# Performance work log

Hardware: AMD Instinct MI355X
Metric: run time of the kernel (lower is better)

Reference implementation:

```python
import jax, jax.numpy as jnp
import numpy as np


def setup_inputs() -> dict:
    key = jax.random.key(0)
    ks = jax.random.split(key, 10)
    B, C, H = 128, 768, 12
    d = C // H
    t_h = t_w = 8
    s_h = s_w = 16
    Nt = t_h * t_w * 2          # 128 template tokens
    Ns = s_h * s_w + 4          # 260 search tokens
    N = Nt + Ns                 # 388
    s = 0.02
    return {
        "x": jax.random.normal(ks[0], (B, N, C), jnp.float32),
        "mem": jax.random.normal(ks[1], (B, H, d, d), jnp.float32),
        "z": jnp.ones((B, H, d, 1), jnp.float32),
        "qkv_w": jax.random.normal(ks[2], (3 * C, C), jnp.float32) * s,
        "qkv_b": jnp.zeros((3 * C,), jnp.float32),
        "proj_w": jax.random.normal(ks[3], (C, C), jnp.float32) * s,
        "proj_b": jnp.zeros((C,), jnp.float32),
        "memk_w": jax.random.normal(ks[4], (C, C), jnp.float32) * s,
        "memk_b": jnp.zeros((C,), jnp.float32),
        "memv_w": jax.random.normal(ks[5], (C, C), jnp.float32) * s,
        "memv_b": jnp.zeros((C,), jnp.float32),
        "betas": jax.random.normal(ks[6], (1, H, 1, d), jnp.float32),
        "t_h": t_h, "t_w": t_w, "s_h": s_h, "s_w": s_w,
    }


def reference(x, mem, z, qkv_w, qkv_b, proj_w, proj_b,
              memk_w, memk_b, memv_w, memv_b, betas,
              t_h, t_w, s_h, s_w):
    B, N, C = x.shape
    H = betas.shape[1]
    d = C // H
    Nt = t_h * t_w * 2
    Ns = s_h * s_w + 4
    scale = 1.0 / jnp.sqrt(jnp.float32(d))

    qkv = x @ qkv_w.T + qkv_b                       # [B,N,3C]
    qkv = qkv.reshape(B, N, 3, C)
    q_f, k_f, v_f = qkv[:, :, 0], qkv[:, :, 1], qkv[:, :, 2]  # [B,N,C]

    def heads(t):  # [B,N,C] -> [B,H,N,d]
        return t.reshape(B, -1, H, d).transpose(0, 2, 1, 3)

    q, k, v = heads(q_f), heads(k_f), heads(v_f)

    # memory k/v projections act on the raw (C-dim) search split of k,v
    k_s_mem = heads(k_f[:, Nt:, :] @ memk_w.T + memk_b)  # [B,H,Ns,d]
    v_s_mem = heads(v_f[:, Nt:, :] @ memv_w.T + memv_b)  # [B,H,Ns,d]

    q_mt, q_s = q[:, :, :Nt], q[:, :, Nt:]
    k_mt = k[:, :, :Nt]
    v_mt = v[:, :, :Nt]

    # template self-attention (q_mt only attends to k_mt)
    attn_mt = jax.nn.softmax(jnp.einsum('bhqd,bhkd->bhqk', q_mt, k_mt) * scale, axis=-1)
    x_mt = jnp.einsum('bhqk,bhkd->bhqd', attn_mt, v_mt)          # [B,H,Nt,d]
    x_mt = x_mt.transpose(0, 2, 1, 3).reshape(B, Nt, C)

    # search attends to full sequence
    attn_s = jax.nn.softmax(jnp.einsum('bhqd,bhkd->bhqk', q_s, k) * scale, axis=-1)
    x_s = jnp.einsum('bhqk,bhkd->bhqd', attn_s, v)               # [B,H,Ns,d]

    # linear-attention memory read (ELU feature map)
    sigma_q = jax.nn.elu(q_s) + 1.0                              # [B,H,Ns,d]
    att_mem = (sigma_q @ mem) / (sigma_q @ z)                    # [B,H,Ns,d]

    # delta-rule memory update
    sigma_k = jax.nn.elu(k_s_mem) + 1.0                          # [B,H,Ns,d]
    zz = jnp.sum(sigma_k, axis=-2, keepdims=True).swapaxes(-2, -1)  # [B,H,d,1]
    pred = (sigma_k @ mem) / (sigma_k @ z)                       # [B,H,Ns,d]
    mem_new = mem + jnp.einsum('bhnd,bhne->bhde', sigma_k, v_s_mem - pred)
    z_new = z + zz

    beta = jax.nn.sigmoid(betas)                                 # [1,H,1,d]
    x_s = beta * att_mem + (1.0 - beta) * x_s
    x_s = x_s.transpose(0, 2, 1, 3).reshape(B, Ns, C)

    out = jnp.concatenate([x_mt, x_s], axis=1) @ proj_w.T + proj_b
    return out, mem_new, z_new
```

## Files before the change

### kernel.cpp

```cpp
#include <hip/hip_runtime.h>

typedef unsigned short u16;
typedef __attribute__((ext_vector_type(8))) short  vbf8;
typedef __attribute__((ext_vector_type(4))) float  vf4;

#define B_   128
#define N_   388
#define NT   128
#define NS   260
#define C_   768
#define H_   12
#define D_   64
#define K3   2304

#define QKV_LEN  114425856ll
#define KSM_LEN  25559040ll
#define CAT_LEN  38141952ll
#define MEM_LEN  6291456ll

#define SPS  288
#define SWT_LEN 28311552ll

#define WOFF_QKV  0ll
#define WOFF_MEMK 1769472ll
#define WOFF_MEMV 2359296ll
#define WOFF_PROJ 2949120ll
#define WTOT     3538944ll
__device__ __align__(16) u16 g_wbf[3538944];

__device__ __forceinline__ float bf2f(u16 u) {
    union { unsigned int i; float f; } v; v.i = ((unsigned int)u) << 16; return v.f;
}
__device__ __forceinline__ u16 f2bf(float f) {
    union { float f; unsigned int i; } v; v.f = f;
    unsigned int r = v.i + 0x7fffu + ((v.i >> 16) & 1u);
    return (u16)(r >> 16);
}
__device__ __forceinline__ float elu1(float x) { return x > 0.f ? x + 1.f : __expf(x); }

__device__ __forceinline__ void gload_lds16(const u16* g, u16* l) {
    __builtin_amdgcn_global_load_lds(
        (const __attribute__((address_space(1))) unsigned int*)g,
        (__attribute__((address_space(3))) unsigned int*)l, 16, 0, 0);
}

__global__ __launch_bounds__(256) void convert_bf16(
    const float* __restrict__ src, u16* __restrict__ dst, long long n)
{
    long long i0 = ((long long)blockIdx.x * 256 + threadIdx.x) * 8;
    long long stride = (long long)gridDim.x * 256 * 8;
    for (long long i = i0; i < n; i += stride) {
        float4 a = *(const float4*)(src + i);
        float4 b = *(const float4*)(src + i + 4);
        ushort4 u1; u1.x = f2bf(a.x); u1.y = f2bf(a.y); u1.z = f2bf(a.z); u1.w = f2bf(a.w);
        ushort4 u2; u2.x = f2bf(b.x); u2.y = f2bf(b.y); u2.z = f2bf(b.z); u2.w = f2bf(b.w);
        *(ushort4*)(dst + i)     = u1;
        *(ushort4*)(dst + i + 4) = u2;
    }
}

__global__ __launch_bounds__(256) void convert_wbf_all(
    const float* __restrict__ s0, const float* __restrict__ s1,
    const float* __restrict__ s2, const float* __restrict__ s3)
{
    long long i = ((long long)blockIdx.x * 256 + threadIdx.x) * 8;
    if (i >= WTOT) return;
    const float* src; long long off;
    if (i < WOFF_MEMK)      { src = s0; off = i; }
    else if (i < WOFF_MEMV) { src = s1; off = i - WOFF_MEMK; }
    else if (i < WOFF_PROJ) { src = s2; off = i - WOFF_MEMV; }
    else                    { src = s3; off = i - WOFF_PROJ; }
    float4 a = *(const float4*)(src + off);
    float4 b = *(const float4*)(src + off + 4);
    ushort4 u1; u1.x = f2bf(a.x); u1.y = f2bf(a.y); u1.z = f2bf(a.z); u1.w = f2bf(a.w);
    ushort4 u2; u2.x = f2bf(b.x); u2.y = f2bf(b.y); u2.z = f2bf(b.z); u2.w = f2bf(b.w);
    *(ushort4*)(g_wbf + i)     = u1;
    *(ushort4*)(g_wbf + i + 4) = u2;
}

__global__ __launch_bounds__(256) void memT_kernel(
    const float* __restrict__ memin, u16* __restrict__ memT)
{
    __shared__ float ml[64 * 65];
    int bh = blockIdx.x, t = threadIdx.x;
    const float* src = memin + (long long)bh * 4096;
#pragma unroll
    for (int i = 0; i < 16; i++) {
        int idx = i * 256 + t;
        ml[(idx >> 6) * 65 + (idx & 63)] = src[idx];
    }
    __syncthreads();
    u16* dst = memT + (long long)bh * 4096;
#pragma unroll
    for (int i = 0; i < 16; i++) {
        int o = i * 256 + t;
        int dout = o >> 6, din = o & 63;
        dst[o] = f2bf(ml[din * 65 + dout]);
    }
}

template<int CF32>
__global__ __launch_bounds__(256) void gemm_mfma(
    const u16* __restrict__ A, long long off0, int rows_per_b,
    long long stride_b, long long stride_r,
    long long w_off, const float* __restrict__ bias,
    void* __restrict__ Cv, int Nout, int nbx)
{
    __shared__ __align__(16) u16 lds[2][2][4096];

    const u16* W = g_wbf + w_off;
    int t = threadIdx.x;

    int wg = blockIdx.x;
    wg = (wg & 7) * ((int)gridDim.x >> 3) + (wg >> 3);
    int m0 = (wg / nbx) * 128;
    int n0 = (wg % nbx) * 128;

    int lane = t & 63, w = t >> 6;
    int w512 = w * 512;

    int srow  = t >> 2;
    int scol  = (((t & 3) ^ ((t >> 3) & 3))) * 8;
    long long aoff0, aoff1;
    {
        int g1 = m0 + srow, g2 = g1 + 64;
        int b1 = g1 / rows_per_b, j1 = g1 - b1 * rows_per_b;
        int b2 = g2 / rows_per_b, j2 = g2 - b2 * rows_per_b;
        aoff0 = off0 + (long long)b1 * stride_b + (long long)j1 * stride_r + scol;
        aoff1 = off0 + (long long)b2 * stride_b + (long long)j2 * stride_r + scol;
    }
    const u16* wp0 = W + (long long)(n0 + srow) * 768 + scol;
    const u16* wp1 = W + (long long)(n0 + srow + 64) * 768 + scol;

    int lr = lane & 15, kg = lane >> 4;
    int wm = w >> 1, wn = w & 1;
    int aslot = (kg ^ ((lr >> 1) & 3)) * 8;
    int abase = (wm * 64 + lr) * 32 + aslot;
    int bbase = (wn * 64 + lr) * 32 + aslot;

    vf4 acc[4][4];
#pragma unroll
    for (int i = 0; i < 4; i++)
#pragma unroll
        for (int j = 0; j < 4; j++) acc[i][j] = vf4{0.f, 0.f, 0.f, 0.f};

    auto stage = [&](int buf, int kt) {
        gload_lds16(A + aoff0 + kt, &lds[buf][0][w512]);
        gload_lds16(A + aoff1 + kt, &lds[buf][0][2048 + w512]);
        gload_lds16(wp0 + kt,       &lds[buf][1][w512]);
        gload_lds16(wp1 + kt,       &lds[buf][1][2048 + w512]);
    };

    stage(0, 0);
    __syncthreads();

    int cur = 0;
    for (int kt = 0; kt < 768; kt += 32) {
        if (kt != 736) stage(cur ^ 1, kt + 32);

        vbf8 af[4], bf[4];
#pragma unroll
        for (int f = 0; f < 4; f++) {
            af[f] = *(const vbf8*)&lds[cur][0][abase + f * 512];
            bf[f] = *(const vbf8*)&lds[cur][1][bbase + f * 512];
        }
#pragma unroll
        for (int i = 0; i < 4; i++)
#pragma unroll
            for (int j = 0; j < 4; j++)
                acc[i][j] = __builtin_amdgcn_mfma_f32_16x16x32_bf16(
                    af[i], bf[j], acc[i][j], 0, 0, 0);

        __syncthreads();
        cur ^= 1;
    }

    if (!CF32) {
        u16* ct = &lds[0][0][0];
#pragma unroll
        for (int i = 0; i < 4; i++)
#pragma unroll
            for (int j = 0; j < 4; j++) {
                int col = wn * 64 + j * 16 + lr;
                float bb = bias[n0 + col];
#pragma unroll
                for (int r = 0; r < 4; r++)
                    ct[(wm * 64 + i * 16 + kg * 4 + r) * 128 + col] =
                        f2bf(acc[i][j][r] + bb);
            }
        __syncthreads();
        int col0 = (t & 15) * 8;
#pragma unroll
        for (int rr = 0; rr < 8; rr++) {
            int row_l = rr * 16 + (t >> 4);
            vbf8 v = *(const vbf8*)&ct[row_l * 128 + col0];
            *(vbf8*)((u16*)Cv + (long long)(m0 + row_l) * Nout + n0 + col0) = v;
        }
    } else {
        float* cf = (float*)&lds[0][0][0];
#pragma unroll
        for (int p = 0; p < 2; p++) {
            if (wm == p) {
#pragma unroll
                for (int i = 0; i < 4; i++)
#pragma unroll
                    for (int j = 0; j < 4; j++) {
                        int col = wn * 64 + j * 16 + lr;
                        float bb = bias[n0 + col];
#pragma unroll
                        for (int r = 0; r < 4; r++)
                            cf[(i * 16 + kg * 4 + r) * 128 + col] =
                                acc[i][j][r] + bb;
                    }
            }
            __syncthreads();
            int col0 = (t & 15) * 8;
#pragma unroll
            for (int rr = 0; rr < 4; rr++) {
                int row_l = rr * 16 + (t >> 4);
                float4 v0 = *(const float4*)&cf[row_l * 128 + col0];
                float4 v1 = *(const float4*)&cf[row_l * 128 + col0 + 4];
                float* dst = (float*)Cv + (long long)(m0 + p * 64 + row_l) * Nout + n0 + col0;
                *(float4*)dst = v0;
                *(float4*)(dst + 4) = v1;
            }
            __syncthreads();
        }
    }
}

#define SKP 416
#define VTS 424
__global__ __launch_bounds__(512) void attn_s_mfma(
    const u16* __restrict__ qkv, const u16* __restrict__ memT,
    const float* __restrict__ zin, const float* __restrict__ betas,
    u16* __restrict__ concat)
{
    __shared__ __align__(16) u16 Kl[SKP * 64];
    __shared__ __align__(16) u16 Vt[64 * VTS];
    __shared__ __align__(16) u16 Pl[8][16 * 40];
    __shared__ float red[8][16];

    int bh = blockIdx.x;
    int b = bh / H_, h = bh % H_;
    int t = threadIdx.x, lane = t & 63, w = t >> 6;
    int lr = lane & 15, q4 = lane >> 4;

    {
        int key0 = t >> 3;
        int d0 = (t & 7) * 8;
        for (int kp = 0; kp < SKP; kp += 64) {
            int key = kp + key0;
            if (key < SKP) {
                vbf8 kv, vv;
#pragma unroll
                for (int u = 0; u < 8; u++) { ((short*)&kv)[u] = 0; ((short*)&vv)[u] = 0; }
                if (key < N_) {
                    const u16* base = qkv + ((long long)(b * N_ + key)) * K3 + h * D_;
                    kv = *(const vbf8*)(base + C_ + d0);
                    vv = *(const vbf8*)(base + 2 * C_ + d0);
                }
                *(vbf8*)((char*)Kl + ((key * 128 + d0 * 2) ^ ((key & 7) << 4))) = kv;
#pragma unroll
                for (int u = 0; u < 8; u++) Vt[(d0 + u) * VTS + key] = ((u16*)&vv)[u];
            }
        }
    }
    __syncthreads();

    const float* zp = zin + bh * 64;
    const u16* mtb = memT + (long long)bh * 4096;

    for (int s = w; s < 17; s += 8) {
        int qtok = NT + s * 16 + lr;
        if (qtok > N_ - 1) qtok = N_ - 1;
        const u16* qbase = qkv + ((long long)(b * N_ + qtok)) * K3 + h * D_;
        vbf8 qf0 = *(const vbf8*)(qbase + q4 * 8);
        vbf8 qf1 = *(const vbf8*)(qbase + 32 + q4 * 8);

        vbf8 qs0, qs1;
#pragma unroll
        for (int j = 0; j < 8; j++) {
            ((u16*)&qs0)[j] = f2bf(bf2f(((u16*)&qf0)[j]) * 0.125f);
            ((u16*)&qs1)[j] = f2bf(bf2f(((u16*)&qf1)[j]) * 0.125f);
        }

        vf4 S[13][2];
#pragma unroll
        for (int kt = 0; kt < 13; kt++) {
#pragma unroll
            for (int ks = 0; ks < 2; ks++) {
                int krow = kt * 32 + ks * 16 + lr;
                int swz = (krow & 7) << 4;
                vbf8 b0 = *(const vbf8*)((char*)Kl + ((krow * 128 + q4 * 16) ^ swz));
                vbf8 b1 = *(const vbf8*)((char*)Kl + ((krow * 128 + 64 + q4 * 16) ^ swz));
                vf4 z4 = vf4{0.f, 0.f, 0.f, 0.f};
                vf4 sv = __builtin_amdgcn_mfma_f32_16x16x32_bf16(qs0, b0, z4, 0, 0, 0);
                S[kt][ks] = __builtin_amdgcn_mfma_f32_16x16x32_bf16(qs1, b1, sv, 0, 0, 0);
            }
        }
#pragma unroll
        for (int ks = 0; ks < 2; ks++)
#pragma unroll
            for (int r = 0; r < 4; r++)
                if (ks * 16 + lr >= 4) S[12][ks][r] = -1e30f;

        float mx[4];
#pragma unroll
        for (int r = 0; r < 4; r++) mx[r] = S[0][0][r];
#pragma unroll
        for (int kt = 0; kt < 13; kt++)
#pragma unroll
            for (int ks = 0; ks < 2; ks++)
#pragma unroll
                for (int r = 0; r < 4; r++) mx[r] = fmaxf(mx[r], S[kt][ks][r]);
#pragma unroll
        for (int off = 1; off <= 8; off <<= 1)
#pragma unroll
            for (int r = 0; r < 4; r++) mx[r] = fmaxf(mx[r], __shfl_xor(mx[r], off));

        float l[4] = {0.f, 0.f, 0.f, 0.f};
#pragma unroll
        for (int kt = 0; kt < 13; kt++)
#pragma unroll
            for (int ks = 0; ks < 2; ks++)
#pragma unroll
                for (int r = 0; r < 4; r++) {
                    float p = __expf(S[kt][ks][r] - mx[r]);
                    S[kt][ks][r] = p;
                    l[r] += p;
                }
#pragma unroll
        for (int off = 1; off <= 8; off <<= 1)
#pragma unroll
            for (int r = 0; r < 4; r++) l[r] += __shfl_xor(l[r], off);

        vf4 accO[4];
#pragma unroll
        for (int dc = 0; dc < 4; dc++) accO[dc] = vf4{0.f, 0.f, 0.f, 0.f};
#pragma unroll
        for (int kt = 0; kt < 13; kt++) {
            u16* pw = Pl[w];
#pragma unroll
            for (int ks = 0; ks < 2; ks++)
#pragma unroll
                for (int r = 0; r < 4; r++)
                    pw[(q4 * 4 + r) * 40 + ks * 16 + lr] = f2bf(S[kt][ks][r]);
            vbf8 pf = *(const vbf8*)&Pl[w][lr * 40 + q4 * 8];
#pragma unroll
            for (int dc = 0; dc < 4; dc++) {
                vbf8 vf_ = *(const vbf8*)&Vt[(dc * 16 + lr) * VTS + kt * 32 + q4 * 8];
                accO[dc] = __builtin_amdgcn_mfma_f32_16x16x32_bf16(pf, vf_, accO[dc], 0, 0, 0);
            }
        }

        float invl[4];
#pragma unroll
        for (int r = 0; r < 4; r++) invl[r] = 1.f / l[r];

        vbf8 sq0, sq1;
        float dpart = 0.f;
#pragma unroll
        for (int j = 0; j < 8; j++) {
            float s0 = elu1(bf2f(((u16*)&qf0)[j]));
            float s1 = elu1(bf2f(((u16*)&qf1)[j]));
            ((u16*)&sq0)[j] = f2bf(s0);
            ((u16*)&sq1)[j] = f2bf(s1);
            dpart += s0 * zp[q4 * 8 + j] + s1 * zp[32 + q4 * 8 + j];
        }
        dpart += __shfl_xor(dpart, 16);
        dpart += __shfl_xor(dpart, 32);
        if (q4 == 0) red[w][lr] = dpart;

        vf4 am[4];
#pragma unroll
        for (int dc = 0; dc < 4; dc++) {
            vbf8 b0 = *(const vbf8*)(mtb + (dc * 16 + lr) * 64 + q4 * 8);
            vbf8 b1 = *(const vbf8*)(mtb + (dc * 16 + lr) * 64 + 32 + q4 * 8);
            vf4 z4 = vf4{0.f, 0.f, 0.f, 0.f};
            vf4 a = __builtin_amdgcn_mfma_f32_16x16x32_bf16(sq0, b0, z4, 0, 0, 0);
            am[dc] = __builtin_amdgcn_mfma_f32_16x16x32_bf16(sq1, b1, a, 0, 0, 0);
        }
        float den[4];
#pragma unroll
        for (int r = 0; r < 4; r++) den[r] = 1.f / red[w][q4 * 4 + r];

#pragma unroll
        for (int dc = 0; dc < 4; dc++) {
            float bb = betas[h * D_ + dc * 16 + lr];
            float beta = 1.f / (1.f + __expf(-bb));
#pragma unroll
            for (int r = 0; r < 4; r++) {
                int qs = s * 16 + q4 * 4 + r;
                if (qs < NS) {
                    float o = beta * (am[dc][r] * den[r]) +
                              (1.f - beta) * (accO[dc][r] * invl[r]);
                    concat[((long long)(b * N_ + NT + qs)) * C_ + h * D_ + dc * 16 + lr] = f2bf(o);
                }
            }
        }
    }
}

#define MTS 136
__global__ __launch_bounds__(512) void attn_mt_mfma(
    const u16* __restrict__ qkv, u16* __restrict__ concat)
{
    __shared__ __align__(16) u16 Kl[NT * 64];
    __shared__ __align__(16) u16 Vt[64 * MTS];
    __shared__ __align__(16) u16 Pl[8][16 * 40];

    int bh = blockIdx.x;
    int b = bh / H_, h = bh % H_;
    int t = threadIdx.x, lane = t & 63, w = t >> 6;
    int lr = lane & 15, q4 = lane >> 4;

    {
        int key0 = t >> 3;
        int d0 = (t & 7) * 8;
#pragma unroll
        for (int kp = 0; kp < NT; kp += 64) {
            int key = kp + key0;
            const u16* base = qkv + ((long long)(b * N_ + key)) * K3 + h * D_;
            vbf8 kv = *(const vbf8*)(base + C_ + d0);
            vbf8 vv = *(const vbf8*)(base + 2 * C_ + d0);
            *(vbf8*)((char*)Kl + ((key * 128 + d0 * 2) ^ ((key & 7) << 4))) = kv;
#pragma unroll
            for (int u = 0; u < 8; u++) Vt[(d0 + u) * MTS + key] = ((u16*)&vv)[u];
        }
    }
    __syncthreads();

    int qtok = w * 16 + lr;
    const u16* qbase = qkv + ((long long)(b * N_ + qtok)) * K3 + h * D_;
    vbf8 qf0 = *(const vbf8*)(qbase + q4 * 8);
    vbf8 qf1 = *(const vbf8*)(qbase + 32 + q4 * 8);
    vbf8 qs0, qs1;
#pragma unroll
    for (int j = 0; j < 8; j++) {
        ((u16*)&qs0)[j] = f2bf(bf2f(((u16*)&qf0)[j]) * 0.125f);
        ((u16*)&qs1)[j] = f2bf(bf2f(((u16*)&qf1)[j]) * 0.125f);
    }

    vf4 S[4][2];
#pragma unroll
    for (int kt = 0; kt < 4; kt++) {
#pragma unroll
        for (int ks = 0; ks < 2; ks++) {
            int krow = kt * 32 + ks * 16 + lr;
            int swz = (krow & 7) << 4;
            vbf8 b0 = *(const vbf8*)((char*)Kl + ((krow * 128 + q4 * 16) ^ swz));
            vbf8 b1 = *(const vbf8*)((char*)Kl + ((krow * 128 + 64 + q4 * 16) ^ swz));
            vf4 z4 = vf4{0.f, 0.f, 0.f, 0.f};
            vf4 sv = __builtin_amdgcn_mfma_f32_16x16x32_bf16(qs0, b0, z4, 0, 0, 0);
            S[kt][ks] = __builtin_amdgcn_mfma_f32_16x16x32_bf16(qs1, b1, sv, 0, 0, 0);
        }
    }

    float mx[4];
#pragma unroll
    for (int r = 0; r < 4; r++) mx[r] = S[0][0][r];
#pragma unroll
    for (int kt = 0; kt < 4; kt++)
#pragma unroll
        for (int ks = 0; ks < 2; ks++)
#pragma unroll
            for (int r = 0; r < 4; r++) mx[r] = fmaxf(mx[r], S[kt][ks][r]);
#pragma unroll
    for (int off = 1; off <= 8; off <<= 1)
#pragma unroll
        for (int r = 0; r < 4; r++) mx[r] = fmaxf(mx[r], __shfl_xor(mx[r], off));

    float l[4] = {0.f, 0.f, 0.f, 0.f};
#pragma unroll
    for (int kt = 0; kt < 4; kt++)
#pragma unroll
        for (int ks = 0; ks < 2; ks++)
#pragma unroll
            for (int r = 0; r < 4; r++) {
                float p = __expf(S[kt][ks][r] - mx[r]);
                S[kt][ks][r] = p;
                l[r] += p;
            }
#pragma unroll
    for (int off = 1; off <= 8; off <<= 1)
#pragma unroll
        for (int r = 0; r < 4; r++) l[r] += __shfl_xor(l[r], off);

    vf4 accO[4];
#pragma unroll
    for (int dc = 0; dc < 4; dc++) accO[dc] = vf4{0.f, 0.f, 0.f, 0.f};
#pragma unroll
    for (int kt = 0; kt < 4; kt++) {
        u16* pw = Pl[w];
#pragma unroll
        for (int ks = 0; ks < 2; ks++)
#pragma unroll
            for (int r = 0; r < 4; r++)
                pw[(q4 * 4 + r) * 40 + ks * 16 + lr] = f2bf(S[kt][ks][r]);
        vbf8 pf = *(const vbf8*)&Pl[w][lr * 40 + q4 * 8];
#pragma unroll
        for (int dc = 0; dc < 4; dc++) {
            vbf8 vf_ = *(const vbf8*)&Vt[(dc * 16 + lr) * MTS + kt * 32 + q4 * 8];
            accO[dc] = __builtin_amdgcn_mfma_f32_16x16x32_bf16(pf, vf_, accO[dc], 0, 0, 0);
        }
    }

    float invl[4];
#pragma unroll
    for (int r = 0; r < 4; r++) invl[r] = 1.f / l[r];

    int qt0 = w * 16;
#pragma unroll
    for (int dc = 0; dc < 4; dc++)
#pragma unroll
        for (int r = 0; r < 4; r++) {
            int row = qt0 + q4 * 4 + r;
            concat[((long long)(b * N_ + row)) * C_ + h * D_ + dc * 16 + lr] =
                f2bf(accO[dc][r] * invl[r]);
        }
}

__global__ __launch_bounds__(512) void sigma_pred_mfma(
    const u16* __restrict__ ksm, const u16* __restrict__ vsm,
    const u16* __restrict__ memT, const float* __restrict__ zin,
    u16* __restrict__ sigT, u16* __restrict__ wT,
    float* __restrict__ z_out)
{
    __shared__ u16 sigLDS[8][64][18];
    __shared__ u16 wLDS[8][64][18];
    __shared__ float red[8][16];
    __shared__ float zpart[8][64];
    __shared__ float zlds[64];

    int bh = blockIdx.x;
    int b = bh / H_, h = bh % H_;
    int t = threadIdx.x, lane = t & 63, w = t >> 6;
    int lr = lane & 15, q4 = lane >> 4;

    if (t < 64) zlds[t] = zin[bh * 64 + t];
    __syncthreads();

    const u16* mtb = memT + (long long)bh * 4096;
    float zacc[16];
#pragma unroll
    for (int j = 0; j < 16; j++) zacc[j] = 0.f;

    for (int s = w; s < 18; s += 8) {
        int n0 = s * 16;
        int nrow = n0 + lr;
        bool vrow = nrow < NS;
        int nclamp = vrow ? nrow : NS - 1;
        const u16* kbase = ksm + ((long long)(b * NS + nclamp)) * C_ + h * D_;
        vbf8 k0 = *(const vbf8*)(kbase + q4 * 8);
        vbf8 k1 = *(const vbf8*)(kbase + 32 + q4 * 8);

        vbf8 sq0, sq1;
        float dpart = 0.f;
#pragma unroll
        for (int j = 0; j < 8; j++) {
            float s0 = vrow ? elu1(bf2f(((u16*)&k0)[j])) : 0.f;
            float s1 = vrow ? elu1(bf2f(((u16*)&k1)[j])) : 0.f;
            ((u16*)&sq0)[j] = f2bf(s0);
            ((u16*)&sq1)[j] = f2bf(s1);
            zacc[j]     += s0;
            zacc[8 + j] += s1;
            dpart += s0 * zlds[q4 * 8 + j] + s1 * zlds[32 + q4 * 8 + j];
        }
        dpart += __shfl_xor(dpart, 16);
        dpart += __shfl_xor(dpart, 32);
        if (q4 == 0) red[w][lr] = dpart;

#pragma unroll
        for (int j = 0; j < 8; j++) {
            sigLDS[w][q4 * 8 + j][lr]      = ((u16*)&sq0)[j];
            sigLDS[w][32 + q4 * 8 + j][lr] = ((u16*)&sq1)[j];
        }

        vf4 am[4];
#pragma unroll
        for (int dc = 0; dc < 4; dc++) {
            vbf8 b0 = *(const vbf8*)(mtb + (dc * 16 + lr) * 64 + q4 * 8);
            vbf8 b1 = *(const vbf8*)(mtb + (dc * 16 + lr) * 64 + 32 + q4 * 8);
            vf4 z4 = vf4{0.f, 0.f, 0.f, 0.f};
            vf4 a = __builtin_amdgcn_mfma_f32_16x16x32_bf16(sq0, b0, z4, 0, 0, 0);
            am[dc] = __builtin_amdgcn_mfma_f32_16x16x32_bf16(sq1, b1, a, 0, 0, 0);
        }
        float rden[4];
#pragma unroll
        for (int r = 0; r < 4; r++) rden[r] = 1.f / red[w][q4 * 4 + r];

#pragma unroll
        for (int dc = 0; dc < 4; dc++) {
            int e = dc * 16 + lr;
#pragma unroll
            for (int r = 0; r < 4; r++) {
                int nn = n0 + q4 * 4 + r;
                float wv = 0.f;
                if (nn < NS) {
                    float pv = am[dc][r] * rden[r];
                    wv = bf2f(vsm[((long long)(b * NS + nn)) * C_ + h * D_ + e]) - pv;
                }
                wLDS[w][e][q4 * 4 + r] = f2bf(wv);
            }
        }

        {
            long long dst = ((long long)bh * 64 + lane) * SPS + n0;
            unsigned pk[8];
#pragma unroll
            for (int j2 = 0; j2 < 8; j2++)
                pk[j2] = (unsigned)sigLDS[w][lane][2 * j2] |
                         ((unsigned)sigLDS[w][lane][2 * j2 + 1] << 16);
            *(uint4*)(sigT + dst)     = uint4{pk[0], pk[1], pk[2], pk[3]};
            *(uint4*)(sigT + dst + 8) = uint4{pk[4], pk[5], pk[6], pk[7]};
#pragma unroll
            for (int j2 = 0; j2 < 8; j2++)
                pk[j2] = (unsigned)wLDS[w][lane][2 * j2] |
                         ((unsigned)wLDS[w][lane][2 * j2 + 1] << 16);
            *(uint4*)(wT + dst)     = uint4{pk[0], pk[1], pk[2], pk[3]};
            *(uint4*)(wT + dst + 8) = uint4{pk[4], pk[5], pk[6], pk[7]};
        }
    }

#pragma unroll
    for (int off = 1; off <= 8; off <<= 1)
#pragma unroll
        for (int j = 0; j < 16; j++) zacc[j] += __shfl_xor(zacc[j], off);
    if (lr == 0) {
#pragma unroll
        for (int j = 0; j < 8; j++) {
            zpart[w][q4 * 8 + j]      = zacc[j];
            zpart[w][32 + q4 * 8 + j] = zacc[8 + j];
        }
    }
    __syncthreads();
    if (t < 64) {
        float tot = 0.f;
#pragma unroll
        for (int ww = 0; ww < 8; ww++) tot += zpart[ww][t];
        z_out[bh * 64 + t] = zlds[t] + tot;
    }
}

__global__ __launch_bounds__(64) void mem_update_mfma(
    const u16* __restrict__ sigT, const u16* __restrict__ wT,
    const float* __restrict__ memin, float* __restrict__ mem_out)
{
    int bh = blockIdx.x;
    int lane = threadIdx.x;
    int lr = lane & 15, q4 = lane >> 4;

    const u16* sb = sigT + (long long)bh * 64 * SPS;
    const u16* wb = wT   + (long long)bh * 64 * SPS;

    vf4 acc[4][4];
#pragma unroll
    for (int i = 0; i < 4; i++)
#pragma unroll
        for (int j = 0; j < 4; j++) acc[i][j] = vf4{0.f, 0.f, 0.f, 0.f};

    for (int kt = 0; kt < SPS; kt += 32) {
        vbf8 af[4], bf[4];
#pragma unroll
        for (int i = 0; i < 4; i++)
            af[i] = *(const vbf8*)(sb + (long long)(i * 16 + lr) * SPS + kt + q4 * 8);
#pragma unroll
        for (int j = 0; j < 4; j++)
            bf[j] = *(const vbf8*)(wb + (long long)(j * 16 + lr) * SPS + kt + q4 * 8);
#pragma unroll
        for (int i = 0; i < 4; i++)
#pragma unroll
            for (int j = 0; j < 4; j++)
                acc[i][j] = __builtin_amdgcn_mfma_f32_16x16x32_bf16(
                    af[i], bf[j], acc[i][j], 0, 0, 0);
    }

    long long mb = (long long)bh * 4096;
#pragma unroll
    for (int i = 0; i < 4; i++)
#pragma unroll
        for (int j = 0; j < 4; j++)
#pragma unroll
            for (int r = 0; r < 4; r++) {
                int d = i * 16 + q4 * 4 + r;
                int e = j * 16 + lr;
                mem_out[mb + d * 64 + e] = memin[mb + d * 64 + e] + acc[i][j][r];
            }
}

extern "C" void kernel_launch(void* const* d_in, const int* in_sizes, int n_in,
                              void* d_out, int out_size, void* d_ws, size_t ws_size,
                              hipStream_t stream)
{
    const float* x      = (const float*)d_in[0];
    const float* mem    = (const float*)d_in[1];
    const float* z      = (const float*)d_in[2];
    const float* qkv_w  = (const float*)d_in[3];
    const float* qkv_b  = (const float*)d_in[4];
    const float* proj_w = (const float*)d_in[5];
    const float* proj_b = (const float*)d_in[6];
    const float* memk_w = (const float*)d_in[7];
    const float* memk_b = (const float*)d_in[8];
    const float* memv_w = (const float*)d_in[9];
    const float* memv_b = (const float*)d_in[10];
    const float* betas  = (const float*)d_in[11];

    u16* ws     = (u16*)d_ws;
    u16* qkv    = ws;
    u16* ksm    = qkv + QKV_LEN;
    u16* vsm    = ksm + KSM_LEN;
    u16* concat = vsm + KSM_LEN;

    float* out     = (float*)d_out;
    float* mem_out = out + CAT_LEN;
    float* z_out   = mem_out + MEM_LEN;

    u16* x_bf = concat;
    u16* memT = (u16*)mem_out;
    u16* sigT = qkv;
    u16* wT   = qkv + SWT_LEN;

    convert_bf16<<<dim3(2048), dim3(256), 0, stream>>>(x, x_bf, CAT_LEN);
    convert_wbf_all<<<dim3(1728), dim3(256), 0, stream>>>(qkv_w, memk_w, memv_w, proj_w);
    memT_kernel<<<dim3(B_ * H_), dim3(256), 0, stream>>>(mem, memT);

    gemm_mfma<0><<<dim3(6984), dim3(256), 0, stream>>>(
        x_bf, 0ll, 49664, 0ll, 768ll, WOFF_QKV, qkv_b, qkv, K3, 18);
    gemm_mfma<0><<<dim3(1560), dim3(256), 0, stream>>>(
        qkv, (long long)(NT * K3 + C_), NS, (long long)N_ * K3, (long long)K3,
        WOFF_MEMK, memk_b, ksm, C_, 6);
    gemm_mfma<0><<<dim3(1560), dim3(256), 0, stream>>>(
        qkv, (long long)(NT * K3 + 2 * C_), NS, (long long)N_ * K3, (long long)K3,
        WOFF_MEMV, memv_b, vsm, C_, 6);
    attn_s_mfma<<<dim3(B_ * H_), dim3(512), 0, stream>>>(
        qkv, memT, z, betas, concat);
    attn_mt_mfma<<<dim3(B_ * H_), dim3(512), 0, stream>>>(qkv, concat);
    sigma_pred_mfma<<<dim3(B_ * H_), dim3(512), 0, stream>>>(
        ksm, vsm, memT, z, sigT, wT, z_out);
    mem_update_mfma<<<dim3(B_ * H_), dim3(64), 0, stream>>>(
        sigT, wT, mem, mem_out);
    gemm_mfma<1><<<dim3(2328), dim3(256), 0, stream>>>(
        concat, 0ll, 49664, 0ll, 768ll, WOFF_PROJ, proj_b, out, C_, 6);
}
```

Before: 1.020 ms.

## Fuse sigma/pred and delta-rule memory update into one kernel via LDS

```diff
diff --git a/kernel.cpp b/kernel.cpp
--- a/kernel.cpp
+++ b/kernel.cpp
@@ -19,7 +19,7 @@
 #define MEM_LEN  6291456ll
 
 #define SPS  288
-#define SWT_LEN 28311552ll
+#define SPL  296
 
 #define WOFF_QKV  0ll
 #define WOFF_MEMK 1769472ll
@@ -120,7 +120,7 @@
     int w512 = w * 512;
 
     int srow  = t >> 2;
-    int scol  = (((t & 3) ^ ((t >> 3) & 3))) * 8;
+    int scol  = (((t & 3) ^ (srow & 3))) * 8;
     long long aoff0, aoff1;
     {
         int g1 = m0 + srow, g2 = g1 + 64;
@@ -134,7 +134,7 @@
 
     int lr = lane & 15, kg = lane >> 4;
     int wm = w >> 1, wn = w & 1;
-    int aslot = (kg ^ ((lr >> 1) & 3)) * 8;
+    int aslot = (kg ^ (lr & 3)) * 8;
     int abase = (wm * 64 + lr) * 32 + aslot;
     int bbase = (wn * 64 + lr) * 32 + aslot;
 
@@ -521,14 +521,14 @@
         }
 }
 
-__global__ __launch_bounds__(512) void sigma_pred_mfma(
+__global__ __launch_bounds__(512) void sigma_pred_mem(
     const u16* __restrict__ ksm, const u16* __restrict__ vsm,
     const u16* __restrict__ memT, const float* __restrict__ zin,
-    u16* __restrict__ sigT, u16* __restrict__ wT,
+    const float* __restrict__ memin, float* __restrict__ mem_out,
     float* __restrict__ z_out)
 {
-    __shared__ u16 sigLDS[8][64][18];
-    __shared__ u16 wLDS[8][64][18];
+    __shared__ __align__(16) u16 sigL[64][SPL];
+    __shared__ __align__(16) u16 wL[64][SPL];
     __shared__ float red[8][16];
     __shared__ float zpart[8][64];
     __shared__ float zlds[64];
@@ -561,21 +561,18 @@
         for (int j = 0; j < 8; j++) {
             float s0 = vrow ? elu1(bf2f(((u16*)&k0)[j])) : 0.f;
             float s1 = vrow ? elu1(bf2f(((u16*)&k1)[j])) : 0.f;
-            ((u16*)&sq0)[j] = f2bf(s0);
-            ((u16*)&sq1)[j] = f2bf(s1);
+            u16 b0 = f2bf(s0), b1 = f2bf(s1);
+            ((u16*)&sq0)[j] = b0;
+            ((u16*)&sq1)[j] = b1;
             zacc[j]     += s0;
             zacc[8 + j] += s1;
             dpart += s0 * zlds[q4 * 8 + j] + s1 * zlds[32 + q4 * 8 + j];
+            sigL[q4 * 8 + j][n0 + lr]      = b0;
+            sigL[32 + q4 * 8 + j][n0 + lr] = b1;
         }
         dpart += __shfl_xor(dpart, 16);
         dpart += __shfl_xor(dpart, 32);
         if (q4 == 0) red[w][lr] = dpart;
-
-#pragma unroll
-        for (int j = 0; j < 8; j++) {
-            sigLDS[w][q4 * 8 + j][lr]      = ((u16*)&sq0)[j];
-            sigLDS[w][32 + q4 * 8 + j][lr] = ((u16*)&sq1)[j];
-        }
 
         vf4 am[4];
 #pragma unroll
@@ -601,25 +598,8 @@
                     float pv = am[dc][r] * rden[r];
                     wv = bf2f(vsm[((long long)(b * NS + nn)) * C_ + h * D_ + e]) - pv;
                 }
-                wLDS[w][e][q4 * 4 + r] = f2bf(wv);
-            }
-        }
-
-        {
-            long long dst = ((long long)bh * 64 + lane) * SPS + n0;
-            unsigned pk[8];
-#pragma unroll
-            for (int j2 = 0; j2 < 8; j2++)
-                pk[j2] = (unsigned)sigLDS[w][lane][2 * j2] |
-                         ((unsigned)sigLDS[w][lane][2 * j2 + 1] << 16);
-            *(uint4*)(sigT + dst)     = uint4{pk[0], pk[1], pk[2], pk[3]};
-            *(uint4*)(sigT + dst + 8) = uint4{pk[4], pk[5], pk[6], pk[7]};
-#pragma unroll
-            for (int j2 = 0; j2 < 8; j2++)
-                pk[j2] = (unsigned)wLDS[w][lane][2 * j2] |
-                         ((unsigned)wLDS[w][lane][2 * j2 + 1] << 16);
-            *(uint4*)(wT + dst)     = uint4{pk[0], pk[1], pk[2], pk[3]};
-            *(uint4*)(wT + dst + 8) = uint4{pk[4], pk[5], pk[6], pk[7]};
+                wL[e][n0 + q4 * 4 + r] = f2bf(wv);
+            }
         }
     }
 
@@ -635,58 +615,33 @@
         }
     }
     __syncthreads();
+
     if (t < 64) {
         float tot = 0.f;
 #pragma unroll
         for (int ww = 0; ww < 8; ww++) tot += zpart[ww][t];
         z_out[bh * 64 + t] = zlds[t] + tot;
     }
-}
-
-__global__ __launch_bounds__(64) void mem_update_mfma(
-    const u16* __restrict__ sigT, const u16* __restrict__ wT,
-    const float* __restrict__ memin, float* __restrict__ mem_out)
-{
-    int bh = blockIdx.x;
-    int lane = threadIdx.x;
-    int lr = lane & 15, q4 = lane >> 4;
-
-    const u16* sb = sigT + (long long)bh * 64 * SPS;
-    const u16* wb = wT   + (long long)bh * 64 * SPS;
-
-    vf4 acc[4][4];
-#pragma unroll
-    for (int i = 0; i < 4; i++)
-#pragma unroll
-        for (int j = 0; j < 4; j++) acc[i][j] = vf4{0.f, 0.f, 0.f, 0.f};
-
-    for (int kt = 0; kt < SPS; kt += 32) {
-        vbf8 af[4], bf[4];
-#pragma unroll
-        for (int i = 0; i < 4; i++)
-            af[i] = *(const vbf8*)(sb + (long long)(i * 16 + lr) * SPS + kt + q4 * 8);
-#pragma unroll
-        for (int j = 0; j < 4; j++)
-            bf[j] = *(const vbf8*)(wb + (long long)(j * 16 + lr) * SPS + kt + q4 * 8);
-#pragma unroll
-        for (int i = 0; i < 4; i++)
-#pragma unroll
-            for (int j = 0; j < 4; j++)
-                acc[i][j] = __builtin_amdgcn_mfma_f32_16x16x32_bf16(
-                    af[i], bf[j], acc[i][j], 0, 0, 0);
-    }
 
     long long mb = (long long)bh * 4096;
 #pragma unroll
-    for (int i = 0; i < 4; i++)
-#pragma unroll
-        for (int j = 0; j < 4; j++)
-#pragma unroll
-            for (int r = 0; r < 4; r++) {
-                int d = i * 16 + q4 * 4 + r;
-                int e = j * 16 + lr;
-                mem_out[mb + d * 64 + e] = memin[mb + d * 64 + e] + acc[i][j][r];
-            }
+    for (int p = 0; p < 2; p++) {
+        int tid2 = w * 2 + p;
+        int i = tid2 >> 2, j = tid2 & 3;
+        vf4 acc = vf4{0.f, 0.f, 0.f, 0.f};
+#pragma unroll
+        for (int kt = 0; kt < SPS; kt += 32) {
+            vbf8 af = *(const vbf8*)&sigL[i * 16 + lr][kt + q4 * 8];
+            vbf8 bf = *(const vbf8*)&wL[j * 16 + lr][kt + q4 * 8];
+            acc = __builtin_amdgcn_mfma_f32_16x16x32_bf16(af, bf, acc, 0, 0, 0);
+        }
+        int e = j * 16 + lr;
+#pragma unroll
+        for (int r = 0; r < 4; r++) {
+            int dd = i * 16 + q4 * 4 + r;
+            mem_out[mb + dd * 64 + e] = memin[mb + dd * 64 + e] + acc[r];
+        }
+    }
 }
 
 extern "C" void kernel_launch(void* const* d_in, const int* in_sizes, int n_in,
@@ -717,9 +672,7 @@
     float* z_out   = mem_out + MEM_LEN;
 
     u16* x_bf = concat;
-    u16* memT = (u16*)mem_out;
-    u16* sigT = qkv;
-    u16* wT   = qkv + SWT_LEN;
+    u16* memT = (u16*)out;
 
     convert_bf16<<<dim3(2048), dim3(256), 0, stream>>>(x, x_bf, CAT_LEN);
     convert_wbf_all<<<dim3(1728), dim3(256), 0, stream>>>(qkv_w, memk_w, memv_w, proj_w);
@@ -736,10 +689,8 @@
     attn_s_mfma<<<dim3(B_ * H_), dim3(512), 0, stream>>>(
         qkv, memT, z, betas, concat);
     attn_mt_mfma<<<dim3(B_ * H_), dim3(512), 0, stream>>>(qkv, concat);
-    sigma_pred_mfma<<<dim3(B_ * H_), dim3(512), 0, stream>>>(
-        ksm, vsm, memT, z, sigT, wT, z_out);
-    mem_update_mfma<<<dim3(B_ * H_), dim3(64), 0, stream>>>(
-        sigT, wT, mem, mem_out);
+    sigma_pred_mem<<<dim3(B_ * H_), dim3(512), 0, stream>>>(
+        ksm, vsm, memT, z, mem, mem_out, z_out);
     gemm_mfma<1><<<dim3(2328), dim3(256), 0, stream>>>(
         concat, 0ll, 49664, 0ll, 768ll, WOFF_PROJ, proj_b, out, C_, 6);
 }
```

New measurement: 887.3 us. 1.15x faster.
